# Performance work log

Hardware: AMD Instinct MI355X
Metric: run time of the kernel (lower is better)

Reference implementation:

```python
import jax, jax.numpy as jnp
import numpy as np

N = 50000        # nodes
E = 800000       # edges (avg degree 16)
OBS = 128        # observation_dim
HID = 64         # hidden_dim (per head)
H1 = 4           # heads in conv1
ACT = 32         # action_dim
NEG_SLOPE = 0.2  # GATv2 default negative_slope


def setup_inputs() -> dict:
    key = jax.random.key(0)
    ks = jax.random.split(key, 10)
    s = 0.05
    x = jax.random.normal(ks[0], (N, OBS), jnp.float32)
    edge_index = jax.random.randint(ks[1], (2, E), 0, N, dtype=jnp.int32)
    # conv1: GATv2Conv(OBS -> HID, heads=4, concat=True)
    W1l = jax.random.normal(ks[2], (OBS, H1 * HID), jnp.float32) * s  # lin_l (source)
    W1r = jax.random.normal(ks[3], (OBS, H1 * HID), jnp.float32) * s  # lin_r (target)
    att1 = jax.random.normal(ks[4], (H1, HID), jnp.float32) * s
    b1 = jnp.zeros((H1 * HID,), jnp.float32)
    # conv2: GATv2Conv(H1*HID -> ACT, heads=1, concat=False)
    W2l = jax.random.normal(ks[5], (H1 * HID, ACT), jnp.float32) * s
    W2r = jax.random.normal(ks[6], (H1 * HID, ACT), jnp.float32) * s
    att2 = jax.random.normal(ks[7], (1, ACT), jnp.float32) * s
    b2 = jnp.zeros((ACT,), jnp.float32)
    return {"x": x, "edge_index": edge_index, "W1l": W1l, "W1r": W1r,
            "att1": att1, "b1": b1, "W2l": W2l, "W2r": W2r,
            "att2": att2, "b2": b2}


def gatv2_layer(x, Wl, Wr, att, bias, src, dst, heads, out_ch, concat):
    """PyG GATv2Conv (add_self_loops=False, share_weights=False)."""
    n = x.shape[0]
    xl = (x @ Wl).reshape(n, heads, out_ch)  # source transform
    xr = (x @ Wr).reshape(n, heads, out_ch)  # target transform
    e = xl[src] + xr[dst]                    # [E, H, C] gathered messages
    g = jnp.where(e > 0, e, NEG_SLOPE * e)   # LeakyReLU
    logits = jnp.einsum('ehc,hc->eh', g, att)  # [E, H]
    # segment softmax over incoming edges of each destination node
    m = jax.ops.segment_max(logits, dst, num_segments=n)      # [N, H]
    ex = jnp.exp(logits - m[dst])
    denom = jax.ops.segment_sum(ex, dst, num_segments=n)      # [N, H]
    alpha = ex / denom[dst]                                   # [E, H]
    out = jax.ops.segment_sum(xl[src] * alpha[:, :, None], dst, num_segments=n)
    out = out.reshape(n, heads * out_ch) if concat else out.mean(axis=1)
    return out + bias


def reference(x, edge_index, W1l, W1r, att1, b1, W2l, W2r, att2, b2):
    src, dst = edge_index[0], edge_index[1]
    h = jax.nn.relu(gatv2_layer(x, W1l, W1r, att1, b1, src, dst, H1, HID, True))
    out = gatv2_layer(h, W2l, W2r, att2, b2, src, dst, 1, ACT, False)
    return out
```

## Files before the change

kernel.cpp:

```cpp
#include <hip/hip_runtime.h>
#include <hip/hip_bf16.h>
#include <math.h>


#define OBS 128
#define HID 64
#define H1 4
#define C1 256
#define ACT 32
#define PAD 64
#define NEG_SLOPE 0.2f
#define LOG2E 1.4426950408889634f
#define CAP 6144
#define AGGB 2048

typedef __attribute__((ext_vector_type(2))) _Float16 h2;
typedef __attribute__((ext_vector_type(8))) _Float16 half8;
typedef __attribute__((ext_vector_type(4))) float f32x4;

__device__ inline h2 bc_h2(unsigned u) { return __builtin_bit_cast(h2, u); }
__device__ inline unsigned bc_u(h2 v) { return __builtin_bit_cast(unsigned, v); }
__device__ inline h2 lrelu2(h2 e) {
  const h2 k = {(_Float16)NEG_SLOPE, (_Float16)NEG_SLOPE};
  return __builtin_elementwise_max(e, e * k);
}

__global__ void prep0(const float* __restrict__ W1l, const float* __restrict__ W1r,
                      const float* __restrict__ W2l, const float* __restrict__ W2r,
                      _Float16* __restrict__ W1t, _Float16* __restrict__ W2t,
                      unsigned* __restrict__ bucketCursor) {
  int i = blockIdx.x * 256 + threadIdx.x;
  if (i < 256) bucketCursor[i] = 0;
  if (i < 512 * 128) {
    int n = i >> 7, k = i & 127;
    float v = (n < C1) ? W1l[k * C1 + n] : W1r[k * C1 + (n - C1)];
    W1t[i] = (_Float16)v;
  }
  int j = i - 512 * 128;
  if (j >= 0 && j < 64 * 256) {
    int n = j >> 8, c = j & 255;
    float v = (n < ACT) ? W2l[c * ACT + n] : W2r[c * ACT + (n - ACT)];
    W2t[j] = (_Float16)v;
  }
}

__global__ __launch_bounds__(256) void gemm1_sc(
    const float* __restrict__ xf,
    const _Float16* __restrict__ W1t,
    _Float16* __restrict__ XLh,
    _Float16* __restrict__ XRh,
    int M,
    const int* __restrict__ src, const int* __restrict__ dst,
    unsigned* __restrict__ bcur, unsigned* __restrict__ sorted,
    int E, int ept) {
  const int LDK = 136;
  __shared__ _Float16 As[128 * 136];
  __shared__ _Float16 Bs[128 * 136];
  __shared__ unsigned cnt[256];
  __shared__ unsigned lbase[256];
  __shared__ unsigned lrank[256];

  const int tid = threadIdx.x;

  cnt[tid] = 0;
  lrank[tid] = 0;
  __syncthreads();
  int ebase = blockIdx.x * ept * 256;
  for (int r = 0; r < ept; ++r) {
    int e = ebase + r * 256 + tid;
    if (e < E) atomicAdd(&cnt[dst[e] >> 8], 1u);
  }
  __syncthreads();
  {
    unsigned c = cnt[tid];
    lbase[tid] = c ? atomicAdd(&bcur[tid], c) : 0u;
  }
  __syncthreads();
  for (int r = 0; r < ept; ++r) {
    int e = ebase + r * 256 + tid;
    if (e < E) {
      int d = dst[e];
      int b = d >> 8;
      unsigned rk = atomicAdd(&lrank[b], 1u);
      unsigned off = lbase[b] + rk;
      if (off < CAP)
        sorted[(size_t)b * CAP + off] =
            ((unsigned)(d & 255) << 16) | (unsigned)src[e];
    }
  }

  const int lane = tid & 63;
  const int wid = tid >> 6;
  const int wm = (wid & 1) * 64, wn = (wid >> 1) * 64;
  const int rowBase = blockIdx.x * 128;
  const int l15 = lane & 15, lq = lane >> 4;

#pragma unroll
  for (int cc = 0; cc < 8; ++cc) {
    int q = cc * 256 + tid;
    int r = q >> 4;
    int kc = (q & 15) * 8;
    int grow = rowBase + r;
    float4 f0 = make_float4(0.f, 0.f, 0.f, 0.f), f1 = f0;
    if (grow < M) {
      f0 = *(const float4*)(xf + (size_t)grow * 128 + kc);
      f1 = *(const float4*)(xf + (size_t)grow * 128 + kc + 4);
    }
    h2 p0 = {(_Float16)f0.x, (_Float16)f0.y};
    h2 p1 = {(_Float16)f0.z, (_Float16)f0.w};
    h2 p2 = {(_Float16)f1.x, (_Float16)f1.y};
    h2 p3 = {(_Float16)f1.z, (_Float16)f1.w};
    *(int4*)(As + r * LDK + kc) = make_int4(bc_u(p0), bc_u(p1), bc_u(p2), bc_u(p3));
  }
#pragma unroll
  for (int cc = 0; cc < 8; ++cc) {
    int q = cc * 256 + tid;
    int r = q >> 4;
    int kc = (q & 15) * 8;
    *(int4*)(Bs + r * LDK + kc) = *(const int4*)(W1t + (size_t)r * 128 + kc);
  }
  __syncthreads();

  for (int cb = 0; cb < 4; ++cb) {
    f32x4 acc[4][4];
#pragma unroll
    for (int i = 0; i < 4; ++i)
#pragma unroll
      for (int j = 0; j < 4; ++j) acc[i][j] = (f32x4){0.f, 0.f, 0.f, 0.f};

#pragma unroll
    for (int ks = 0; ks < 4; ++ks) {
      half8 af[4], bf[4];
#pragma unroll
      for (int t = 0; t < 4; ++t) {
        af[t] = *(const half8*)(As + (wm + t * 16 + l15) * LDK + ks * 32 + lq * 8);
        bf[t] = *(const half8*)(Bs + (wn + t * 16 + l15) * LDK + ks * 32 + lq * 8);
      }
#pragma unroll
      for (int mt = 0; mt < 4; ++mt)
#pragma unroll
        for (int nt = 0; nt < 4; ++nt)
          acc[mt][nt] = __builtin_amdgcn_mfma_f32_16x16x32_f16(
              af[mt], bf[nt], acc[mt][nt], 0, 0, 0);
    }

    _Float16* outp = (cb < 2) ? XLh : XRh;
    int colBase = (cb & 1) * 128;
#pragma unroll
    for (int mt = 0; mt < 4; ++mt) {
#pragma unroll
      for (int r = 0; r < 4; ++r) {
        int row = rowBase + wm + mt * 16 + lq * 4 + r;
        if (row >= M) continue;
#pragma unroll
        for (int nt = 0; nt < 4; ++nt) {
          int col = colBase + wn + nt * 16 + l15;
          outp[(size_t)row * C1 + col] = (_Float16)acc[mt][nt][r];
        }
      }
    }

    if (cb < 3) {
      __syncthreads();
#pragma unroll
      for (int cc = 0; cc < 8; ++cc) {
        int q = cc * 256 + tid;
        int r = q >> 4;
        int kc = (q & 15) * 8;
        *(int4*)(Bs + r * LDK + kc) =
            *(const int4*)(W1t + (size_t)((cb + 1) * 128 + r) * 128 + kc);
      }
      __syncthreads();
    }
  }
}

__global__ __launch_bounds__(256) void bcsr_k(const unsigned* __restrict__ sorted,
                                              const unsigned* __restrict__ bucketCursor,
                                              unsigned short* __restrict__ esrc_p,
                                              int* __restrict__ cursor, int N) {
  __shared__ unsigned cnt2[256];
  int b = blockIdx.x;
  int t = threadIdx.x;
  cnt2[t] = 0;
  __syncthreads();
  unsigned total = bucketCursor[b];
  if (total > CAP) total = CAP;
  const unsigned* sp = sorted + (size_t)b * CAP;
  for (unsigned e = t; e < total; e += 256) {
    unsigned u = sp[e];
    unsigned dl = u >> 16;
    unsigned slot = atomicAdd(&cnt2[dl], 1u);
    if (slot < PAD)
      esrc_p[((size_t)((b << 8) + (int)dl) << 6) + slot] =
          (unsigned short)(u & 0xFFFFu);
  }
  __syncthreads();
  int node = (b << 8) + t;
  if (node < N) cursor[node] = (int)cnt2[t];
}

__global__ __launch_bounds__(256) void agg1(const _Float16* __restrict__ XLh,
                                            const _Float16* XRh,
                                            const float* __restrict__ att1,
                                            const float* __restrict__ b1,
                                            const int* __restrict__ degp,
                                            const unsigned short* __restrict__ esrc_p,
                                            _Float16* Hh, int n_nodes) {
  int wave = threadIdx.x >> 6;
  int lane = threadIdx.x & 63;
  int n = blockIdx.x * 4 + wave;
  if (n >= n_nodes) return;
  int sl = lane & 31;
  int half = lane >> 5;
  int c8 = sl * 8;

  const char* XLb = (const char*)XLh + c8 * 2;
  int4 xru = *(const int4*)((const char*)XRh + ((size_t)n << 9) + c8 * 2);
  h2 xr[4] = {bc_h2(xru.x), bc_h2(xru.y), bc_h2(xru.z), bc_h2(xru.w)};
  const float* ap = att1 + (c8 >> 6) * HID + (c8 & 63);
  float4 a0 = *(const float4*)ap;
  float4 a1 = *(const float4*)(ap + 4);
  h2 av[4] = {{(_Float16)(a0.x * LOG2E), (_Float16)(a0.y * LOG2E)},
              {(_Float16)(a0.z * LOG2E), (_Float16)(a0.w * LOG2E)},
              {(_Float16)(a1.x * LOG2E), (_Float16)(a1.y * LOG2E)},
              {(_Float16)(a1.z * LOG2E), (_Float16)(a1.w * LOG2E)}};

  int d = min(degp[n], PAD);
  const unsigned short* ep = esrc_p + ((size_t)n << 6);
  float l = 0.f;
  h2 acc[4];
#pragma unroll
  for (int k = 0; k < 4; ++k) acc[k] = (h2){(_Float16)0.f, (_Float16)0.f};

  int base = 0;
  for (; base + 16 <= d; base += 16) {
    int4 u[8];
#pragma unroll
    for (int t = 0; t < 8; ++t) {
      int s = ep[base + 2 * t + half];
      u[t] = *(const int4*)(XLb + ((size_t)s << 9));
    }
    float c[8];
#pragma unroll
    for (int t = 0; t < 8; ++t) {
      h2 xa = bc_h2(u[t].x), xb = bc_h2(u[t].y), xc = bc_h2(u[t].z), xd = bc_h2(u[t].w);
      float cc = __builtin_amdgcn_fdot2(lrelu2(xa + xr[0]), av[0], 0.f, false);
      cc = __builtin_amdgcn_fdot2(lrelu2(xb + xr[1]), av[1], cc, false);
      cc = __builtin_amdgcn_fdot2(lrelu2(xc + xr[2]), av[2], cc, false);
      cc = __builtin_amdgcn_fdot2(lrelu2(xd + xr[3]), av[3], cc, false);
      c[t] = cc;
    }
#pragma unroll
    for (int t = 0; t < 8; ++t) {
      c[t] += __shfl_xor(c[t], 1);
      c[t] += __shfl_xor(c[t], 2);
      c[t] += __shfl_xor(c[t], 4);
    }
#pragma unroll
    for (int t = 0; t < 8; ++t) {
      float p = __builtin_amdgcn_exp2f(c[t]);
      l += p;
      _Float16 ph = (_Float16)p;
      h2 w = {ph, ph};
      acc[0] = acc[0] + w * bc_h2(u[t].x);
      acc[1] = acc[1] + w * bc_h2(u[t].y);
      acc[2] = acc[2] + w * bc_h2(u[t].z);
      acc[3] = acc[3] + w * bc_h2(u[t].w);
    }
  }
  for (; base + 4 <= d; base += 4) {
    int s0 = ep[base + half];
    int s1 = ep[base + 2 + half];
    int4 u0 = *(const int4*)(XLb + ((size_t)s0 << 9));
    int4 u1 = *(const int4*)(XLb + ((size_t)s1 << 9));
    h2 x0[4] = {bc_h2(u0.x), bc_h2(u0.y), bc_h2(u0.z), bc_h2(u0.w)};
    h2 x1[4] = {bc_h2(u1.x), bc_h2(u1.y), bc_h2(u1.z), bc_h2(u1.w)};
    float c0 = 0.f, c1 = 0.f;
#pragma unroll
    for (int k = 0; k < 4; ++k) {
      c0 = __builtin_amdgcn_fdot2(lrelu2(x0[k] + xr[k]), av[k], c0, false);
      c1 = __builtin_amdgcn_fdot2(lrelu2(x1[k] + xr[k]), av[k], c1, false);
    }
    c0 += __shfl_xor(c0, 1); c1 += __shfl_xor(c1, 1);
    c0 += __shfl_xor(c0, 2); c1 += __shfl_xor(c1, 2);
    c0 += __shfl_xor(c0, 4); c1 += __shfl_xor(c1, 4);
    float p0 = __builtin_amdgcn_exp2f(c0);
    float p1 = __builtin_amdgcn_exp2f(c1);
    l += p0 + p1;
    _Float16 q0 = (_Float16)p0, q1 = (_Float16)p1;
    h2 w0 = {q0, q0}, w1 = {q1, q1};
#pragma unroll
    for (int k = 0; k < 4; ++k) acc[k] = acc[k] + w0 * x0[k] + w1 * x1[k];
  }
  if (base < d) {
    int e0 = base + half, e1 = base + 2 + half;
    bool v0 = e0 < d, v1 = e1 < d;
    int s0 = ep[v0 ? e0 : 0];
    int s1 = ep[v1 ? e1 : 0];
    int4 u0 = *(const int4*)(XLb + ((size_t)s0 << 9));
    int4 u1 = *(const int4*)(XLb + ((size_t)s1 << 9));
    h2 x0[4] = {bc_h2(u0.x), bc_h2(u0.y), bc_h2(u0.z), bc_h2(u0.w)};
    h2 x1[4] = {bc_h2(u1.x), bc_h2(u1.y), bc_h2(u1.z), bc_h2(u1.w)};
    float c0 = 0.f, c1 = 0.f;
#pragma unroll
    for (int k = 0; k < 4; ++k) {
      c0 = __builtin_amdgcn_fdot2(lrelu2(x0[k] + xr[k]), av[k], c0, false);
      c1 = __builtin_amdgcn_fdot2(lrelu2(x1[k] + xr[k]), av[k], c1, false);
    }
    c0 += __shfl_xor(c0, 1); c1 += __shfl_xor(c1, 1);
    c0 += __shfl_xor(c0, 2); c1 += __shfl_xor(c1, 2);
    c0 += __shfl_xor(c0, 4); c1 += __shfl_xor(c1, 4);
    float p0 = v0 ? __builtin_amdgcn_exp2f(c0) : 0.f;
    float p1 = v1 ? __builtin_amdgcn_exp2f(c1) : 0.f;
    l += p0 + p1;
    _Float16 q0 = (_Float16)p0, q1 = (_Float16)p1;
    h2 w0 = {q0, q0}, w1 = {q1, q1};
#pragma unroll
    for (int k = 0; k < 4; ++k) acc[k] = acc[k] + w0 * x0[k] + w1 * x1[k];
  }

  l += __shfl_xor(l, 32);
#pragma unroll
  for (int k = 0; k < 4; ++k) {
    unsigned o = __shfl_xor((int)bc_u(acc[k]), 32);
    acc[k] = acc[k] + bc_h2(o);
  }

  float inv = (d > 0) ? 1.f / l : 0.f;
  if (half == 0) {
    float4 b0 = *(const float4*)(b1 + c8);
    float4 b3 = *(const float4*)(b1 + c8 + 4);
    float o0 = fmaxf((float)acc[0][0] * inv + b0.x, 0.f);
    float o1 = fmaxf((float)acc[0][1] * inv + b0.y, 0.f);
    float o2 = fmaxf((float)acc[1][0] * inv + b0.z, 0.f);
    float o3 = fmaxf((float)acc[1][1] * inv + b0.w, 0.f);
    float o4 = fmaxf((float)acc[2][0] * inv + b3.x, 0.f);
    float o5 = fmaxf((float)acc[2][1] * inv + b3.y, 0.f);
    float o6 = fmaxf((float)acc[3][0] * inv + b3.z, 0.f);
    float o7 = fmaxf((float)acc[3][1] * inv + b3.w, 0.f);
    h2 q0 = {(_Float16)o0, (_Float16)o1};
    h2 q1 = {(_Float16)o2, (_Float16)o3};
    h2 q2 = {(_Float16)o4, (_Float16)o5};
    h2 q3 = {(_Float16)o6, (_Float16)o7};
    *(int4*)((char*)Hh + ((size_t)n << 9) + c8 * 2) =
        make_int4(bc_u(q0), bc_u(q1), bc_u(q2), bc_u(q3));
  }
}

__global__ __launch_bounds__(256) void gemm_mfma2(
    const _Float16* __restrict__ Hh,
    const _Float16* __restrict__ W2t,
    _Float16* __restrict__ H2h,
    int M) {
  const int LDK = 136;
  __shared__ _Float16 As[128 * 136];
  __shared__ _Float16 Bs[64 * 136];
  const int tid = threadIdx.x;
  const int lane = tid & 63;
  const int wid = tid >> 6;
  const int wm = (wid & 1) * 64, wn = (wid >> 1) * 32;
  const int rowBase = blockIdx.x * 128;

  f32x4 acc[4][2];
#pragma unroll
  for (int i = 0; i < 4; ++i)
#pragma unroll
    for (int j = 0; j < 2; ++j) acc[i][j] = (f32x4){0.f, 0.f, 0.f, 0.f};

  const int l15 = lane & 15, lq = lane >> 4;

  for (int kb = 0; kb < 256; kb += 128) {
#pragma unroll
    for (int cc = 0; cc < 8; ++cc) {
      int q = cc * 256 + tid;
      int r = q >> 4;
      int kc = (q & 15) * 8;
      int grow = rowBase + r;
      int4 av = make_int4(0, 0, 0, 0);
      if (grow < M) av = *(const int4*)(Hh + (size_t)grow * 256 + kb + kc);
      *(int4*)(As + r * LDK + kc) = av;
    }
#pragma unroll
    for (int cc = 0; cc < 4; ++cc) {
      int q = cc * 256 + tid;
      int r = q >> 4;
      int kc = (q & 15) * 8;
      *(int4*)(Bs + r * LDK + kc) = *(const int4*)(W2t + (size_t)r * 256 + kb + kc);
    }
    __syncthreads();

#pragma unroll
    for (int ks = 0; ks < 4; ++ks) {
      half8 af[4], bf[2];
#pragma unroll
      for (int t = 0; t < 4; ++t)
        af[t] = *(const half8*)(As + (wm + t * 16 + l15) * LDK + ks * 32 + lq * 8);
#pragma unroll
      for (int t = 0; t < 2; ++t)
        bf[t] = *(const half8*)(Bs + (wn + t * 16 + l15) * LDK + ks * 32 + lq * 8);
#pragma unroll
      for (int mt = 0; mt < 4; ++mt)
#pragma unroll
        for (int nt = 0; nt < 2; ++nt)
          acc[mt][nt] = __builtin_amdgcn_mfma_f32_16x16x32_f16(
              af[mt], bf[nt], acc[mt][nt], 0, 0, 0);
    }
    __syncthreads();
  }

#pragma unroll
  for (int mt = 0; mt < 4; ++mt) {
#pragma unroll
    for (int r = 0; r < 4; ++r) {
      int row = rowBase + wm + mt * 16 + lq * 4 + r;
      if (row >= M) continue;
#pragma unroll
      for (int nt = 0; nt < 2; ++nt) {
        int col = wn + nt * 16 + l15;
        H2h[(size_t)row * 64 + col] = (_Float16)acc[mt][nt][r];
      }
    }
  }
}

__global__ __launch_bounds__(256) void agg2(const _Float16* __restrict__ H2h,
                                            const float* __restrict__ att2,
                                            const float* __restrict__ b2,
                                            const int* __restrict__ degp,
                                            const unsigned short* __restrict__ esrc_p,
                                            float* __restrict__ out, int n_nodes) {
  int wave = threadIdx.x >> 6;
  int lane = threadIdx.x & 63;
  int wgid = blockIdx.x * 4 + wave;
  int W = gridDim.x * 4;
  int g = lane >> 3;
  int j = lane & 7;
  int c4 = j * 4;

  const char* Hb = (const char*)H2h + c4 * 2;
  float4 af = *(const float4*)(att2 + c4);
  h2 a0 = {(_Float16)(af.x * LOG2E), (_Float16)(af.y * LOG2E)};
  h2 a1 = {(_Float16)(af.z * LOG2E), (_Float16)(af.w * LOG2E)};
  float4 bb = *(const float4*)(b2 + c4);

  for (int n0 = wgid * 2; n0 < n_nodes; n0 += W * 2) {
    int n1 = n0 + 1;
    bool has1 = n1 < n_nodes;
    int n1s = has1 ? n1 : n0;

    uint2 hru0 = *(const uint2*)((const char*)H2h + ((size_t)n0 << 7) + 64 + c4 * 2);
    uint2 hru1 = *(const uint2*)((const char*)H2h + ((size_t)n1s << 7) + 64 + c4 * 2);
    h2 hr00 = bc_h2(hru0.x), hr01 = bc_h2(hru0.y);
    h2 hr10 = bc_h2(hru1.x), hr11 = bc_h2(hru1.y);

    int d0 = min(degp[n0], PAD);
    int d1 = has1 ? min(degp[n1], PAD) : 0;
    const unsigned short* ep0 = esrc_p + ((size_t)n0 << 6);
    const unsigned short* ep1 = esrc_p + ((size_t)n1s << 6);

    float l0 = 0.f, l1 = 0.f;
    h2 z = {(_Float16)0.f, (_Float16)0.f};
    h2 acc00 = z, acc01 = z, acc10 = z, acc11 = z;

    int dmax = d0 > d1 ? d0 : d1;
    for (int base = 0; base < dmax; base += 16) {
      int eA = base + g, eB = base + 8 + g;
      bool vA0 = eA < d0, vB0 = eB < d0;
      bool vA1 = eA < d1, vB1 = eB < d1;
      int sA0 = ep0[vA0 ? eA : 0];
      int sB0 = ep0[vB0 ? eB : 0];
      int sA1 = ep1[vA1 ? eA : 0];
      int sB1 = ep1[vB1 ? eB : 0];
      uint2 uA0 = *(const uint2*)(Hb + ((size_t)sA0 << 7));
      uint2 uB0 = *(const uint2*)(Hb + ((size_t)sB0 << 7));
      uint2 uA1 = *(const uint2*)(Hb + ((size_t)sA1 << 7));
      uint2 uB1 = *(const uint2*)(Hb + ((size_t)sB1 << 7));
      h2 hA0x = bc_h2(uA0.x), hA0y = bc_h2(uA0.y);
      h2 hB0x = bc_h2(uB0.x), hB0y = bc_h2(uB0.y);
      h2 hA1x = bc_h2(uA1.x), hA1y = bc_h2(uA1.y);
      h2 hB1x = bc_h2(uB1.x), hB1y = bc_h2(uB1.y);
      float cA0 = __builtin_amdgcn_fdot2(lrelu2(hA0x + hr00), a0,
                  __builtin_amdgcn_fdot2(lrelu2(hA0y + hr01), a1, 0.f, false), false);
      float cB0 = __builtin_amdgcn_fdot2(lrelu2(hB0x + hr00), a0,
                  __builtin_amdgcn_fdot2(lrelu2(hB0y + hr01), a1, 0.f, false), false);
      float cA1 = __builtin_amdgcn_fdot2(lrelu2(hA1x + hr10), a0,
                  __builtin_amdgcn_fdot2(lrelu2(hA1y + hr11), a1, 0.f, false), false);
      float cB1 = __builtin_amdgcn_fdot2(lrelu2(hB1x + hr10), a0,
                  __builtin_amdgcn_fdot2(lrelu2(hB1y + hr11), a1, 0.f, false), false);
#pragma unroll
      for (int o = 1; o < 8; o <<= 1) {
        cA0 += __shfl_xor(cA0, o); cB0 += __shfl_xor(cB0, o);
        cA1 += __shfl_xor(cA1, o); cB1 += __shfl_xor(cB1, o);
      }
      float pA0 = vA0 ? __builtin_amdgcn_exp2f(cA0) : 0.f;
      float pB0 = vB0 ? __builtin_amdgcn_exp2f(cB0) : 0.f;
      float pA1 = vA1 ? __builtin_amdgcn_exp2f(cA1) : 0.f;
      float pB1 = vB1 ? __builtin_amdgcn_exp2f(cB1) : 0.f;
      l0 += pA0 + pB0;
      l1 += pA1 + pB1;
      _Float16 qA0 = (_Float16)pA0, qB0 = (_Float16)pB0;
      _Float16 qA1 = (_Float16)pA1, qB1 = (_Float16)pB1;
      h2 wA0 = {qA0, qA0}, wB0 = {qB0, qB0};
      h2 wA1 = {qA1, qA1}, wB1 = {qB1, qB1};
      acc00 = acc00 + wA0 * hA0x + wB0 * hB0x;
      acc01 = acc01 + wA0 * hA0y + wB0 * hB0y;
      acc10 = acc10 + wA1 * hA1x + wB1 * hB1x;
      acc11 = acc11 + wA1 * hA1y + wB1 * hB1y;
    }

#pragma unroll
    for (int o = 8; o < 64; o <<= 1) {
      l0 += __shfl_xor(l0, o);
      l1 += __shfl_xor(l1, o);
      acc00 = acc00 + bc_h2((unsigned)__shfl_xor((int)bc_u(acc00), o));
      acc01 = acc01 + bc_h2((unsigned)__shfl_xor((int)bc_u(acc01), o));
      acc10 = acc10 + bc_h2((unsigned)__shfl_xor((int)bc_u(acc10), o));
      acc11 = acc11 + bc_h2((unsigned)__shfl_xor((int)bc_u(acc11), o));
    }

    if (g == 0) {
      float4 o;
      if (d0 > 0) {
        float inv = 1.f / l0;
        o.x = (float)acc00[0] * inv + bb.x;
        o.y = (float)acc00[1] * inv + bb.y;
        o.z = (float)acc01[0] * inv + bb.z;
        o.w = (float)acc01[1] * inv + bb.w;
      } else {
        o = bb;
      }
      *(float4*)(out + (size_t)n0 * ACT + c4) = o;
    } else if (g == 1 && has1) {
      float4 o;
      if (d1 > 0) {
        float inv = 1.f / l1;
        o.x = (float)acc10[0] * inv + bb.x;
        o.y = (float)acc10[1] * inv + bb.y;
        o.z = (float)acc11[0] * inv + bb.z;
        o.w = (float)acc11[1] * inv + bb.w;
      } else {
        o = bb;
      }
      *(float4*)(out + (size_t)n1 * ACT + c4) = o;
    }
  }
}

extern "C" void kernel_launch(void* const* d_in, const int* in_sizes, int n_in,
                              void* d_out, int out_size, void* d_ws, size_t ws_size,
                              hipStream_t stream) {
  (void)n_in; (void)out_size; (void)ws_size;
  const float* x    = (const float*)d_in[0];
  const int*   ei   = (const int*)d_in[1];
  const float* W1l  = (const float*)d_in[2];
  const float* W1r  = (const float*)d_in[3];
  const float* att1 = (const float*)d_in[4];
  const float* b1   = (const float*)d_in[5];
  const float* W2l  = (const float*)d_in[6];
  const float* W2r  = (const float*)d_in[7];
  const float* att2 = (const float*)d_in[8];
  const float* b2   = (const float*)d_in[9];
  float* out = (float*)d_out;

  const int N = in_sizes[0] / OBS;
  const int E = in_sizes[1] / 2;
  const int* src = ei;
  const int* dst = ei + E;

  _Float16* XLh = (_Float16*)d_ws;
  _Float16* XRh = XLh + (size_t)N * C1;
  _Float16* W1t = XRh + (size_t)N * C1;
  _Float16* W2t = W1t + 512 * 128;
  int* cursor   = (int*)(W2t + 64 * 256);
  unsigned short* esrc_p = (unsigned short*)(cursor + N);
  _Float16* Hh  = XRh;
  _Float16* H2h = XLh;

  int NB = (N + 255) >> 8;
  unsigned* sortedW = (unsigned*)(esrc_p + (size_t)N * PAD);
  unsigned* bcur    = sortedW + (size_t)NB * CAP;

  dim3 b256(256);
  int gemmBlocks = (N + 127) / 128;
  int prepBlocks = (512 * 128 + 64 * 256 + 255) / 256;
  int ept = (E + gemmBlocks * 256 - 1) / (gemmBlocks * 256);
  int aggBlocks = AGGB;
  if (aggBlocks * 8 > N) aggBlocks = (N + 7) / 8;

  prep0<<<prepBlocks, b256, 0, stream>>>(W1l, W1r, W2l, W2r, W1t, W2t, bcur);
  gemm1_sc<<<gemmBlocks, b256, 0, stream>>>(
      x, W1t, XLh, XRh, N, src, dst, bcur, sortedW, E, ept);
  bcsr_k<<<NB, b256, 0, stream>>>(sortedW, bcur, esrc_p, cursor, N);
  agg1<<<(N + 3) / 4, b256, 0, stream>>>(XLh, XRh, att1, b1, cursor, esrc_p, Hh, N);
  gemm_mfma2<<<gemmBlocks, b256, 0, stream>>>(Hh, W2t, H2h, N);
  agg2<<<aggBlocks, b256, 0, stream>>>(H2h, att2, b2, cursor, esrc_p, out, N);
}
```

Baseline: 221.0 us.

## Fuse layer-2 projection GEMM into layer-1 aggregation kernel via shared-memory MFMA

The layer-1 aggregation kernel now writes each block's 4 node outputs into shared memory and immediately multiplies them by W2 with a 16x16x32 MFMA, writing H2 directly. This removes the separate GEMM launch and the global round trip of the 256-wide hidden activations. In exchange, each block uses only 4 of 16 MFMA rows and re-reads W2 from global/cache per block. H2 is moved to the sorted-edge scratch buffer, which is free by then, so XL/XR are no longer overwritten.

```diff
diff --git a/kernel.cpp b/kernel.cpp
--- a/kernel.cpp
+++ b/kernel.cpp
@@ -200,225 +200,177 @@
   if (node < N) cursor[node] = (int)cnt2[t];
 }
 
-__global__ __launch_bounds__(256) void agg1(const _Float16* __restrict__ XLh,
-                                            const _Float16* XRh,
-                                            const float* __restrict__ att1,
-                                            const float* __restrict__ b1,
-                                            const int* __restrict__ degp,
-                                            const unsigned short* __restrict__ esrc_p,
-                                            _Float16* Hh, int n_nodes) {
+__global__ __launch_bounds__(256) void agg1f(const _Float16* __restrict__ XLh,
+                                             const _Float16* __restrict__ XRh,
+                                             const _Float16* __restrict__ W2t,
+                                             const float* __restrict__ att1,
+                                             const float* __restrict__ b1,
+                                             const int* __restrict__ degp,
+                                             const unsigned short* __restrict__ esrc_p,
+                                             _Float16* __restrict__ H2h,
+                                             int n_nodes) {
+  const int LDR = 264;
+  __shared__ _Float16 Hs[16 * LDR];
   int wave = threadIdx.x >> 6;
   int lane = threadIdx.x & 63;
-  int n = blockIdx.x * 4 + wave;
-  if (n >= n_nodes) return;
+  int blockBase = blockIdx.x * 4;
+  int n = blockBase + wave;
   int sl = lane & 31;
   int half = lane >> 5;
   int c8 = sl * 8;
 
-  const char* XLb = (const char*)XLh + c8 * 2;
-  int4 xru = *(const int4*)((const char*)XRh + ((size_t)n << 9) + c8 * 2);
-  h2 xr[4] = {bc_h2(xru.x), bc_h2(xru.y), bc_h2(xru.z), bc_h2(xru.w)};
-  const float* ap = att1 + (c8 >> 6) * HID + (c8 & 63);
-  float4 a0 = *(const float4*)ap;
-  float4 a1 = *(const float4*)(ap + 4);
-  h2 av[4] = {{(_Float16)(a0.x * LOG2E), (_Float16)(a0.y * LOG2E)},
-              {(_Float16)(a0.z * LOG2E), (_Float16)(a0.w * LOG2E)},
-              {(_Float16)(a1.x * LOG2E), (_Float16)(a1.y * LOG2E)},
-              {(_Float16)(a1.z * LOG2E), (_Float16)(a1.w * LOG2E)}};
-
-  int d = min(degp[n], PAD);
-  const unsigned short* ep = esrc_p + ((size_t)n << 6);
-  float l = 0.f;
-  h2 acc[4];
-#pragma unroll
-  for (int k = 0; k < 4; ++k) acc[k] = (h2){(_Float16)0.f, (_Float16)0.f};
-
-  int base = 0;
-  for (; base + 16 <= d; base += 16) {
-    int4 u[8];
-#pragma unroll
-    for (int t = 0; t < 8; ++t) {
-      int s = ep[base + 2 * t + half];
-      u[t] = *(const int4*)(XLb + ((size_t)s << 9));
-    }
-    float c[8];
-#pragma unroll
-    for (int t = 0; t < 8; ++t) {
-      h2 xa = bc_h2(u[t].x), xb = bc_h2(u[t].y), xc = bc_h2(u[t].z), xd = bc_h2(u[t].w);
-      float cc = __builtin_amdgcn_fdot2(lrelu2(xa + xr[0]), av[0], 0.f, false);
-      cc = __builtin_amdgcn_fdot2(lrelu2(xb + xr[1]), av[1], cc, false);
-      cc = __builtin_amdgcn_fdot2(lrelu2(xc + xr[2]), av[2], cc, false);
-      cc = __builtin_amdgcn_fdot2(lrelu2(xd + xr[3]), av[3], cc, false);
-      c[t] = cc;
-    }
-#pragma unroll
-    for (int t = 0; t < 8; ++t) {
-      c[t] += __shfl_xor(c[t], 1);
-      c[t] += __shfl_xor(c[t], 2);
-      c[t] += __shfl_xor(c[t], 4);
-    }
-#pragma unroll
-    for (int t = 0; t < 8; ++t) {
-      float p = __builtin_amdgcn_exp2f(c[t]);
-      l += p;
-      _Float16 ph = (_Float16)p;
-      h2 w = {ph, ph};
-      acc[0] = acc[0] + w * bc_h2(u[t].x);
-      acc[1] = acc[1] + w * bc_h2(u[t].y);
-      acc[2] = acc[2] + w * bc_h2(u[t].z);
-      acc[3] = acc[3] + w * bc_h2(u[t].w);
-    }
-  }
-  for (; base + 4 <= d; base += 4) {
-    int s0 = ep[base + half];
-    int s1 = ep[base + 2 + half];
-    int4 u0 = *(const int4*)(XLb + ((size_t)s0 << 9));
-    int4 u1 = *(const int4*)(XLb + ((size_t)s1 << 9));
-    h2 x0[4] = {bc_h2(u0.x), bc_h2(u0.y), bc_h2(u0.z), bc_h2(u0.w)};
-    h2 x1[4] = {bc_h2(u1.x), bc_h2(u1.y), bc_h2(u1.z), bc_h2(u1.w)};
-    float c0 = 0.f, c1 = 0.f;
+  if (n < n_nodes) {
+    const char* XLb = (const char*)XLh + c8 * 2;
+    int4 xru = *(const int4*)((const char*)XRh + ((size_t)n << 9) + c8 * 2);
+    h2 xr[4] = {bc_h2(xru.x), bc_h2(xru.y), bc_h2(xru.z), bc_h2(xru.w)};
+    const float* ap = att1 + (c8 >> 6) * HID + (c8 & 63);
+    float4 a0 = *(const float4*)ap;
+    float4 a1 = *(const float4*)(ap + 4);
+    h2 av[4] = {{(_Float16)(a0.x * LOG2E), (_Float16)(a0.y * LOG2E)},
+                {(_Float16)(a0.z * LOG2E), (_Float16)(a0.w * LOG2E)},
+                {(_Float16)(a1.x * LOG2E), (_Float16)(a1.y * LOG2E)},
+                {(_Float16)(a1.z * LOG2E), (_Float16)(a1.w * LOG2E)}};
+
+    int d = min(degp[n], PAD);
+    const unsigned short* ep = esrc_p + ((size_t)n << 6);
+    float l = 0.f;
+    h2 acc[4];
+#pragma unroll
+    for (int k = 0; k < 4; ++k) acc[k] = (h2){(_Float16)0.f, (_Float16)0.f};
+
+    int base = 0;
+    for (; base + 16 <= d; base += 16) {
+      int4 u[8];
+#pragma unroll
+      for (int t = 0; t < 8; ++t) {
+        int s = ep[base + 2 * t + half];
+        u[t] = *(const int4*)(XLb + ((size_t)s << 9));
+      }
+      float c[8];
+#pragma unroll
+      for (int t = 0; t < 8; ++t) {
+        h2 xa = bc_h2(u[t].x), xb = bc_h2(u[t].y), xc = bc_h2(u[t].z), xd = bc_h2(u[t].w);
+        float cc = __builtin_amdgcn_fdot2(lrelu2(xa + xr[0]), av[0], 0.f, false);
+        cc = __builtin_amdgcn_fdot2(lrelu2(xb + xr[1]), av[1], cc, false);
+        cc = __builtin_amdgcn_fdot2(lrelu2(xc + xr[2]), av[2], cc, false);
+        cc = __builtin_amdgcn_fdot2(lrelu2(xd + xr[3]), av[3], cc, false);
+        c[t] = cc;
+      }
+#pragma unroll
+      for (int t = 0; t < 8; ++t) {
+        c[t] += __shfl_xor(c[t], 1);
+        c[t] += __shfl_xor(c[t], 2);
+        c[t] += __shfl_xor(c[t], 4);
+      }
+#pragma unroll
+      for (int t = 0; t < 8; ++t) {
+        float p = __builtin_amdgcn_exp2f(c[t]);
+        l += p;
+        _Float16 ph = (_Float16)p;
+        h2 w = {ph, ph};
+        acc[0] = acc[0] + w * bc_h2(u[t].x);
+        acc[1] = acc[1] + w * bc_h2(u[t].y);
+        acc[2] = acc[2] + w * bc_h2(u[t].z);
+        acc[3] = acc[3] + w * bc_h2(u[t].w);
+      }
+    }
+    for (; base + 4 <= d; base += 4) {
+      int s0 = ep[base + half];
+      int s1 = ep[base + 2 + half];
+      int4 u0 = *(const int4*)(XLb + ((size_t)s0 << 9));
+      int4 u1 = *(const int4*)(XLb + ((size_t)s1 << 9));
+      h2 x0[4] = {bc_h2(u0.x), bc_h2(u0.y), bc_h2(u0.z), bc_h2(u0.w)};
+      h2 x1[4] = {bc_h2(u1.x), bc_h2(u1.y), bc_h2(u1.z), bc_h2(u1.w)};
+      float c0 = 0.f, c1 = 0.f;
+#pragma unroll
+      for (int k = 0; k < 4; ++k) {
+        c0 = __builtin_amdgcn_fdot2(lrelu2(x0[k] + xr[k]), av[k], c0, false);
+        c1 = __builtin_amdgcn_fdot2(lrelu2(x1[k] + xr[k]), av[k], c1, false);
+      }
+      c0 += __shfl_xor(c0, 1); c1 += __shfl_xor(c1, 1);
+      c0 += __shfl_xor(c0, 2); c1 += __shfl_xor(c1, 2);
+      c0 += __shfl_xor(c0, 4); c1 += __shfl_xor(c1, 4);
+      float p0 = __builtin_amdgcn_exp2f(c0);
+      float p1 = __builtin_amdgcn_exp2f(c1);
+      l += p0 + p1;
+      _Float16 q0 = (_Float16)p0, q1 = (_Float16)p1;
+      h2 w0 = {q0, q0}, w1 = {q1, q1};
+#pragma unroll
+      for (int k = 0; k < 4; ++k) acc[k] = acc[k] + w0 * x0[k] + w1 * x1[k];
+    }
+    if (base < d) {
+      int e0 = base + half, e1 = base + 2 + half;
+      bool v0 = e0 < d, v1 = e1 < d;
+      int s0 = ep[v0 ? e0 : 0];
+      int s1 = ep[v1 ? e1 : 0];
+      int4 u0 = *(const int4*)(XLb + ((size_t)s0 << 9));
+      int4 u1 = *(const int4*)(XLb + ((size_t)s1 << 9));
+      h2 x0[4] = {bc_h2(u0.x), bc_h2(u0.y), bc_h2(u0.z), bc_h2(u0.w)};
+      h2 x1[4] = {bc_h2(u1.x), bc_h2(u1.y), bc_h2(u1.z), bc_h2(u1.w)};
+      float c0 = 0.f, c1 = 0.f;
+#pragma unroll
+      for (int k = 0; k < 4; ++k) {
+        c0 = __builtin_amdgcn_fdot2(lrelu2(x0[k] + xr[k]), av[k], c0, false);
+        c1 = __builtin_amdgcn_fdot2(lrelu2(x1[k] + xr[k]), av[k], c1, false);
+      }
+      c0 += __shfl_xor(c0, 1); c1 += __shfl_xor(c1, 1);
+      c0 += __shfl_xor(c0, 2); c1 += __shfl_xor(c1, 2);
+      c0 += __shfl_xor(c0, 4); c1 += __shfl_xor(c1, 4);
+      float p0 = v0 ? __builtin_amdgcn_exp2f(c0) : 0.f;
+      float p1 = v1 ? __builtin_amdgcn_exp2f(c1) : 0.f;
+      l += p0 + p1;
+      _Float16 q0 = (_Float16)p0, q1 = (_Float16)p1;
+      h2 w0 = {q0, q0}, w1 = {q1, q1};
+#pragma unroll
+      for (int k = 0; k < 4; ++k) acc[k] = acc[k] + w0 * x0[k] + w1 * x1[k];
+    }
+
+    l += __shfl_xor(l, 32);
 #pragma unroll
     for (int k = 0; k < 4; ++k) {
-      c0 = __builtin_amdgcn_fdot2(lrelu2(x0[k] + xr[k]), av[k], c0, false);
-      c1 = __builtin_amdgcn_fdot2(lrelu2(x1[k] + xr[k]), av[k], c1, false);
-    }
-    c0 += __shfl_xor(c0, 1); c1 += __shfl_xor(c1, 1);
-    c0 += __shfl_xor(c0, 2); c1 += __shfl_xor(c1, 2);
-    c0 += __shfl_xor(c0, 4); c1 += __shfl_xor(c1, 4);
-    float p0 = __builtin_amdgcn_exp2f(c0);
-    float p1 = __builtin_amdgcn_exp2f(c1);
-    l += p0 + p1;
-    _Float16 q0 = (_Float16)p0, q1 = (_Float16)p1;
-    h2 w0 = {q0, q0}, w1 = {q1, q1};
-#pragma unroll
-    for (int k = 0; k < 4; ++k) acc[k] = acc[k] + w0 * x0[k] + w1 * x1[k];
-  }
-  if (base < d) {
-    int e0 = base + half, e1 = base + 2 + half;
-    bool v0 = e0 < d, v1 = e1 < d;
-    int s0 = ep[v0 ? e0 : 0];
-    int s1 = ep[v1 ? e1 : 0];
-    int4 u0 = *(const int4*)(XLb + ((size_t)s0 << 9));
-    int4 u1 = *(const int4*)(XLb + ((size_t)s1 << 9));
-    h2 x0[4] = {bc_h2(u0.x), bc_h2(u0.y), bc_h2(u0.z), bc_h2(u0.w)};
-    h2 x1[4] = {bc_h2(u1.x), bc_h2(u1.y), bc_h2(u1.z), bc_h2(u1.w)};
-    float c0 = 0.f, c1 = 0.f;
-#pragma unroll
-    for (int k = 0; k < 4; ++k) {
-      c0 = __builtin_amdgcn_fdot2(lrelu2(x0[k] + xr[k]), av[k], c0, false);
-      c1 = __builtin_amdgcn_fdot2(lrelu2(x1[k] + xr[k]), av[k], c1, false);
-    }
-    c0 += __shfl_xor(c0, 1); c1 += __shfl_xor(c1, 1);
-    c0 += __shfl_xor(c0, 2); c1 += __shfl_xor(c1, 2);
-    c0 += __shfl_xor(c0, 4); c1 += __shfl_xor(c1, 4);
-    float p0 = v0 ? __builtin_amdgcn_exp2f(c0) : 0.f;
-    float p1 = v1 ? __builtin_amdgcn_exp2f(c1) : 0.f;
-    l += p0 + p1;
-    _Float16 q0 = (_Float16)p0, q1 = (_Float16)p1;
-    h2 w0 = {q0, q0}, w1 = {q1, q1};
-#pragma unroll
-    for (int k = 0; k < 4; ++k) acc[k] = acc[k] + w0 * x0[k] + w1 * x1[k];
-  }
-
-  l += __shfl_xor(l, 32);
-#pragma unroll
-  for (int k = 0; k < 4; ++k) {
-    unsigned o = __shfl_xor((int)bc_u(acc[k]), 32);
-    acc[k] = acc[k] + bc_h2(o);
-  }
-
-  float inv = (d > 0) ? 1.f / l : 0.f;
-  if (half == 0) {
-    float4 b0 = *(const float4*)(b1 + c8);
-    float4 b3 = *(const float4*)(b1 + c8 + 4);
-    float o0 = fmaxf((float)acc[0][0] * inv + b0.x, 0.f);
-    float o1 = fmaxf((float)acc[0][1] * inv + b0.y, 0.f);
-    float o2 = fmaxf((float)acc[1][0] * inv + b0.z, 0.f);
-    float o3 = fmaxf((float)acc[1][1] * inv + b0.w, 0.f);
-    float o4 = fmaxf((float)acc[2][0] * inv + b3.x, 0.f);
-    float o5 = fmaxf((float)acc[2][1] * inv + b3.y, 0.f);
-    float o6 = fmaxf((float)acc[3][0] * inv + b3.z, 0.f);
-    float o7 = fmaxf((float)acc[3][1] * inv + b3.w, 0.f);
-    h2 q0 = {(_Float16)o0, (_Float16)o1};
-    h2 q1 = {(_Float16)o2, (_Float16)o3};
-    h2 q2 = {(_Float16)o4, (_Float16)o5};
-    h2 q3 = {(_Float16)o6, (_Float16)o7};
-    *(int4*)((char*)Hh + ((size_t)n << 9) + c8 * 2) =
-        make_int4(bc_u(q0), bc_u(q1), bc_u(q2), bc_u(q3));
-  }
-}
-
-__global__ __launch_bounds__(256) void gemm_mfma2(
-    const _Float16* __restrict__ Hh,
-    const _Float16* __restrict__ W2t,
-    _Float16* __restrict__ H2h,
-    int M) {
-  const int LDK = 136;
-  __shared__ _Float16 As[128 * 136];
-  __shared__ _Float16 Bs[64 * 136];
-  const int tid = threadIdx.x;
-  const int lane = tid & 63;
-  const int wid = tid >> 6;
-  const int wm = (wid & 1) * 64, wn = (wid >> 1) * 32;
-  const int rowBase = blockIdx.x * 128;
-
-  f32x4 acc[4][2];
-#pragma unroll
-  for (int i = 0; i < 4; ++i)
-#pragma unroll
-    for (int j = 0; j < 2; ++j) acc[i][j] = (f32x4){0.f, 0.f, 0.f, 0.f};
-
-  const int l15 = lane & 15, lq = lane >> 4;
-
-  for (int kb = 0; kb < 256; kb += 128) {
-#pragma unroll
-    for (int cc = 0; cc < 8; ++cc) {
-      int q = cc * 256 + tid;
-      int r = q >> 4;
-      int kc = (q & 15) * 8;
-      int grow = rowBase + r;
-      int4 av = make_int4(0, 0, 0, 0);
-      if (grow < M) av = *(const int4*)(Hh + (size_t)grow * 256 + kb + kc);
-      *(int4*)(As + r * LDK + kc) = av;
-    }
-#pragma unroll
-    for (int cc = 0; cc < 4; ++cc) {
-      int q = cc * 256 + tid;
-      int r = q >> 4;
-      int kc = (q & 15) * 8;
-      *(int4*)(Bs + r * LDK + kc) = *(const int4*)(W2t + (size_t)r * 256 + kb + kc);
-    }
-    __syncthreads();
-
-#pragma unroll
-    for (int ks = 0; ks < 4; ++ks) {
-      half8 af[4], bf[2];
-#pragma unroll
-      for (int t = 0; t < 4; ++t)
-        af[t] = *(const half8*)(As + (wm + t * 16 + l15) * LDK + ks * 32 + lq * 8);
-#pragma unroll
-      for (int t = 0; t < 2; ++t)
-        bf[t] = *(const half8*)(Bs + (wn + t * 16 + l15) * LDK + ks * 32 + lq * 8);
-#pragma unroll
-      for (int mt = 0; mt < 4; ++mt)
-#pragma unroll
-        for (int nt = 0; nt < 2; ++nt)
-          acc[mt][nt] = __builtin_amdgcn_mfma_f32_16x16x32_f16(
-              af[mt], bf[nt], acc[mt][nt], 0, 0, 0);
-    }
-    __syncthreads();
-  }
-
-#pragma unroll
-  for (int mt = 0; mt < 4; ++mt) {
-#pragma unroll
-    for (int r = 0; r < 4; ++r) {
-      int row = rowBase + wm + mt * 16 + lq * 4 + r;
-      if (row >= M) continue;
-#pragma unroll
-      for (int nt = 0; nt < 2; ++nt) {
-        int col = wn + nt * 16 + l15;
-        H2h[(size_t)row * 64 + col] = (_Float16)acc[mt][nt][r];
+      unsigned o = __shfl_xor((int)bc_u(acc[k]), 32);
+      acc[k] = acc[k] + bc_h2(o);
+    }
+
+    float inv = (d > 0) ? 1.f / l : 0.f;
+    if (half == 0) {
+      float4 b0 = *(const float4*)(b1 + c8);
+      float4 b3 = *(const float4*)(b1 + c8 + 4);
+      float o0 = fmaxf((float)acc[0][0] * inv + b0.x, 0.f);
+      float o1 = fmaxf((float)acc[0][1] * inv + b0.y, 0.f);
+      float o2 = fmaxf((float)acc[1][0] * inv + b0.z, 0.f);
+      float o3 = fmaxf((float)acc[1][1] * inv + b0.w, 0.f);
+      float o4 = fmaxf((float)acc[2][0] * inv + b3.x, 0.f);
+      float o5 = fmaxf((float)acc[2][1] * inv + b3.y, 0.f);
+      float o6 = fmaxf((float)acc[3][0] * inv + b3.z, 0.f);
+      float o7 = fmaxf((float)acc[3][1] * inv + b3.w, 0.f);
+      h2 q0 = {(_Float16)o0, (_Float16)o1};
+      h2 q1 = {(_Float16)o2, (_Float16)o3};
+      h2 q2 = {(_Float16)o4, (_Float16)o5};
+      h2 q3 = {(_Float16)o6, (_Float16)o7};
+      *(int4*)(Hs + wave * LDR + c8) =
+          make_int4(bc_u(q0), bc_u(q1), bc_u(q2), bc_u(q3));
+    }
+  }
+
+  __syncthreads();
+
+  {
+    const int l15 = lane & 15, lq = lane >> 4;
+    const int wn = wave * 16;
+    f32x4 acc2 = (f32x4){0.f, 0.f, 0.f, 0.f};
+#pragma unroll
+    for (int ks = 0; ks < 8; ++ks) {
+      half8 af = *(const half8*)(Hs + l15 * LDR + ks * 32 + lq * 8);
+      half8 bf = *(const half8*)(W2t + (size_t)(wn + l15) * 256 + ks * 32 + lq * 8);
+      acc2 = __builtin_amdgcn_mfma_f32_16x16x32_f16(af, bf, acc2, 0, 0, 0);
+    }
+    if (lq == 0) {
+#pragma unroll
+      for (int r = 0; r < 4; ++r) {
+        int ng = blockBase + r;
+        if (ng < n_nodes)
+          H2h[(size_t)ng * 64 + wn + l15] = (_Float16)acc2[r];
       }
     }
   }
@@ -574,12 +526,11 @@
   _Float16* W2t = W1t + 512 * 128;
   int* cursor   = (int*)(W2t + 64 * 256);
   unsigned short* esrc_p = (unsigned short*)(cursor + N);
-  _Float16* Hh  = XRh;
-  _Float16* H2h = XLh;
 
   int NB = (N + 255) >> 8;
   unsigned* sortedW = (unsigned*)(esrc_p + (size_t)N * PAD);
   unsigned* bcur    = sortedW + (size_t)NB * CAP;
+  _Float16* H2h     = (_Float16*)sortedW;
 
   dim3 b256(256);
   int gemmBlocks = (N + 127) / 128;
@@ -592,7 +543,7 @@
   gemm1_sc<<<gemmBlocks, b256, 0, stream>>>(
       x, W1t, XLh, XRh, N, src, dst, bcur, sortedW, E, ept);
   bcsr_k<<<NB, b256, 0, stream>>>(sortedW, bcur, esrc_p, cursor, N);
-  agg1<<<(N + 3) / 4, b256, 0, stream>>>(XLh, XRh, att1, b1, cursor, esrc_p, Hh, N);
-  gemm_mfma2<<<gemmBlocks, b256, 0, stream>>>(Hh, W2t, H2h, N);
+  agg1f<<<(N + 3) / 4, b256, 0, stream>>>(
+      XLh, XRh, W2t, att1, b1, cursor, esrc_p, H2h, N);
   agg2<<<aggBlocks, b256, 0, stream>>>(H2h, att2, b2, cursor, esrc_p, out, N);
 }
```

New measurement: 244.6 us. +10.7%, slower.
